# Kernel tuning notes

Hardware: AMD Instinct MI355X
Metric: run time of the kernel (lower is better)

The kernel has to match this reference:

```python
import jax, jax.numpy as jnp
import numpy as np

# Dims: B batch, CK key dim, CV value dim, NOBJ objects, T memory frames, HxW feature map
B, CK, CV, NOBJ, T, H, W = 1, 64, 512, 2, 2, 64, 64


def setup_inputs() -> dict:
    key = jax.random.key(0)
    k1, k2, k3, k4, k5 = jax.random.split(key, 5)
    return {
        "query_key": jax.random.normal(k1, (B, CK, H, W), jnp.float32),
        "query_selection": jax.random.uniform(k2, (B, CK, H, W), jnp.float32),
        "memory_key": jax.random.normal(k3, (B, CK, T, H, W), jnp.float32),
        "memory_shrinkage": jax.random.uniform(k4, (B, 1, T, H, W), jnp.float32),
        "memory_value": jax.random.normal(k5, (B, NOBJ, CV, T, H, W), jnp.float32),
    }


def reference(query_key, query_selection, memory_key, memory_shrinkage, memory_value):
    b, nobj, cv = memory_value.shape[:3]
    ck = memory_key.shape[1]
    h, w = query_key.shape[-2:]
    hw = h * w
    mk = memory_key.reshape(b, ck, -1)            # (b, ck, N) with N = T*H*W
    ms = memory_shrinkage.reshape(b, -1)          # (b, N)
    qk = query_key.reshape(b, ck, hw)             # (b, ck, hw)
    qe = query_selection.reshape(b, ck, hw)       # (b, ck, hw)
    mv = memory_value.reshape(b, nobj * cv, -1)   # (b, nobj*cv, N)

    # Negative L2 similarity with selection weighting (XMem get_similarity)
    a_sq = jnp.einsum('bcn,bcp->bnp', mk * mk, qe)            # (b, N, hw)
    two_ab = 2.0 * jnp.einsum('bcn,bcp->bnp', mk, qk * qe)    # (b, N, hw)
    b_sq = jnp.sum(qe * qk * qk, axis=1, keepdims=True)       # (b, 1, hw)
    inv_sqrt_ck = np.float32(1.0 / np.sqrt(ck))
    sim = (two_ab - a_sq - b_sq) * ms[:, :, None] * inv_sqrt_ck

    # Softmax over memory slots (dim N), then weighted readout
    aff = jax.nn.softmax(sim, axis=1)                          # (b, N, hw)
    mem = jnp.einsum('bvn,bnp->bvp', mv, aff)                  # (b, nobj*cv, hw)
    return mem.reshape(b, nobj, cv, h, w)
```

## Files before the change

kernel.cpp:

```cpp
#include <hip/hip_runtime.h>
#include <stdint.h>

typedef unsigned short u16;
typedef __attribute__((ext_vector_type(4))) float f32x4;
typedef __attribute__((ext_vector_type(8))) __bf16 bf16x8;
typedef __attribute__((ext_vector_type(4))) unsigned int u32x4;

#define HWPX 4096
#define NMEM 8192
#define CKD  64
#define VROWS 1024

__device__ __forceinline__ u16 f2bf(float x) {
    union { float f; unsigned u; } v; v.f = x;
    unsigned r = v.u + 0x7FFFu + ((v.u >> 16) & 1u);
    return (u16)(r >> 16);
}

__device__ __forceinline__ void gld_lds16(const void* g, void* l) {
    __builtin_amdgcn_global_load_lds(
        (const __attribute__((address_space(1))) uint32_t*)g,
        (__attribute__((address_space(3))) uint32_t*)l, 16, 0, 0);
}

__global__ void prep_qk(const float* __restrict__ qk, const float* __restrict__ qe,
                        const float* __restrict__ mk,
                        u16* __restrict__ Qhat, float* __restrict__ bsq,
                        u16* __restrict__ Khat) {
    const int bx = blockIdx.x;
    const int tid = threadIdx.x;
    if (bx < 16) {
        int p = bx * 256 + tid;
        float acc = 0.f;
        #pragma unroll 4
        for (int c = 0; c < CKD; ++c) {
            float k = qk[c * HWPX + p];
            float e = qe[c * HWPX + p];
            Qhat[p * 128 + c]      = f2bf(k * e);
            Qhat[p * 128 + 64 + c] = f2bf(e);
            acc += e * k * k;
        }
        bsq[p] = acc;
    } else {
        int n = (bx - 16) * 256 + tid;
        #pragma unroll 4
        for (int c = 0; c < CKD; ++c) {
            float m = mk[c * NMEM + n];
            Khat[n * 128 + c]      = f2bf(2.f * m);
            Khat[n * 128 + 64 + c] = f2bf(-m * m);
        }
    }
}

__launch_bounds__(256, 4)
__global__ void gemm1_combo(const u16* __restrict__ Qhat, const u16* __restrict__ Khat,
                            const float* __restrict__ bsq, const float* __restrict__ ms,
                            const float* __restrict__ mv,
                            u16* __restrict__ Pt, float* __restrict__ dpart,
                            u16* __restrict__ mvb, float* __restrict__ outz) {
    const int blk = blockIdx.x;
    const int tid = threadIdx.x;

    if (blk < 512) {
        #pragma unroll 4
        for (int it = 0; it < 16; ++it) {
            int i = blk * 4096 + it * 256 + tid;
            float4 v = ((const float4*)mv)[i];
            u16 o0 = f2bf(v.x), o1 = f2bf(v.y), o2 = f2bf(v.z), o3 = f2bf(v.w);
            unsigned lo = (unsigned)o0 | ((unsigned)o1 << 16);
            unsigned hi = (unsigned)o2 | ((unsigned)o3 << 16);
            ((uint2*)mvb)[i] = make_uint2(lo, hi);
        }
        return;
    }
    if (blk < 768) {
        #pragma unroll 4
        for (int it = 0; it < 16; ++it) {
            int i = (blk - 512) * 4096 + it * 256 + tid;
            ((float4*)outz)[i] = make_float4(0.f, 0.f, 0.f, 0.f);
        }
        return;
    }

    __shared__ __align__(16) u16 smem[17408];
    u16* Qs = smem;
    u16* Ks = smem + 8192;

    const int tile = blk - 768;
    const int pb = tile & 31;
    const int nb = tile >> 5;
    const int p0 = pb * 128;
    const int n0 = nb * 128;

    const int l    = tid & 63;
    const int w    = tid >> 6;
    const int quad = l >> 4;
    const int l15  = l & 15;
    const int wm = w >> 1, wn = w & 1;

    const int rsub = tid >> 3;
    const int csw  = (tid & 7) ^ (rsub & 7);

    f32x4 acc[4][4] = {};

    #pragma unroll
    for (int h = 0; h < 2; ++h) {
        if (h) __syncthreads();
        #pragma unroll
        for (int rnd = 0; rnd < 4; ++rnd)
            gld_lds16(Qhat + (size_t)(p0 + rnd * 32 + rsub) * 128 + h * 64 + csw * 8,
                      Qs + rnd * 2048 + w * 512);
        #pragma unroll
        for (int rnd = 0; rnd < 4; ++rnd)
            gld_lds16(Khat + (size_t)(n0 + rnd * 32 + rsub) * 128 + h * 64 + csw * 8,
                      Ks + rnd * 2048 + w * 512);
        __syncthreads();
        #pragma unroll
        for (int kk = 0; kk < 2; ++kk) {
            bf16x8 a[4], b[4];
            #pragma unroll
            for (int mi = 0; mi < 4; ++mi) {
                int row = wm * 64 + mi * 16 + l15;
                a[mi] = *(const bf16x8*)(Qs + row * 64 + (((kk * 4 + quad) ^ (l15 & 7)) << 3));
            }
            #pragma unroll
            for (int ni = 0; ni < 4; ++ni) {
                int row = wn * 64 + ni * 16 + l15;
                b[ni] = *(const bf16x8*)(Ks + row * 64 + (((kk * 4 + quad) ^ (l15 & 7)) << 3));
            }
            #pragma unroll
            for (int mi = 0; mi < 4; ++mi)
                #pragma unroll
                for (int ni = 0; ni < 4; ++ni)
                    acc[mi][ni] = __builtin_amdgcn_mfma_f32_16x16x32_bf16(a[mi], b[ni], acc[mi][ni], 0, 0, 0);
        }
    }

    float msv[4];
    #pragma unroll
    for (int ni = 0; ni < 4; ++ni)
        msv[ni] = ms[n0 + wn * 64 + ni * 16 + l15] * 0.125f;
    float bsv[4][4];
    #pragma unroll
    for (int mi = 0; mi < 4; ++mi)
        #pragma unroll
        for (int r = 0; r < 4; ++r)
            bsv[mi][r] = bsq[p0 + wm * 64 + mi * 16 + quad * 4 + r];

    __syncthreads();
    u16* Ps = smem;
    float rowsum[4][4] = {};
    #pragma unroll
    for (int mi = 0; mi < 4; ++mi) {
        #pragma unroll
        for (int ni = 0; ni < 4; ++ni) {
            f32x4 v = acc[mi][ni];
            int col = wn * 64 + ni * 16 + l15;
            #pragma unroll
            for (int r = 0; r < 4; ++r) {
                int rowl = wm * 64 + mi * 16 + quad * 4 + r;
                float pv = __expf((v[r] - bsv[mi][r]) * msv[ni]);
                rowsum[mi][r] += pv;
                Ps[rowl * 136 + col] = f2bf(pv);
            }
        }
    }
    #pragma unroll
    for (int mi = 0; mi < 4; ++mi)
        #pragma unroll
        for (int r = 0; r < 4; ++r) {
            float s = rowsum[mi][r];
            s += __shfl_xor(s, 1);
            s += __shfl_xor(s, 2);
            s += __shfl_xor(s, 4);
            s += __shfl_xor(s, 8);
            rowsum[mi][r] = s;
        }
    {
        float myv = 0.f;
        #pragma unroll
        for (int mi = 0; mi < 4; ++mi)
            #pragma unroll
            for (int r = 0; r < 4; ++r)
                if (l15 == mi * 4 + r) myv = rowsum[mi][r];
        int slice = nb * 2 + wn;
        dpart[(size_t)slice * HWPX + p0 + wm * 64 + (l15 >> 2) * 16 + quad * 4 + (l15 & 3)] = myv;
    }
    __syncthreads();

    {
        const size_t dstBase = ((size_t)pb * 64 + nb) * 16384;
        #pragma unroll
        for (int i = 0; i < 8; ++i) {
            int row = i * 16 + (tid >> 4);
            const u32x4* src = (const u32x4*)(Ps + row * 136 + (tid & 15) * 8);
            u32x4* dst = (u32x4*)(Pt + dstBase + row * 128 + (tid & 15) * 8);
            *dst = *src;
        }
    }
}

__launch_bounds__(256, 4)
__global__ void gemm2_kernel(const u16* __restrict__ Ab, const u16* __restrict__ Bt,
                             const float* __restrict__ dpart, float* __restrict__ outacc) {
    __shared__ __align__(16) u16 As[128 * 64];
    __shared__ __align__(16) u16 Bs[128 * 64];

    const int tid  = threadIdx.x;
    const int l    = tid & 63;
    const int w    = tid >> 6;
    const int quad = l >> 4;
    const int l15  = l & 15;
    const int wm = w >> 1, wn = w & 1;

    const int lin = blockIdx.x + (blockIdx.y << 3) + (blockIdx.z << 8);
    const int vb  = (lin >> 3) & 7;
    const int pb  = (lin & 7) | (((lin >> 6) & 3) << 3);
    const int kz  = lin >> 8;
    const int v0 = vb * 128;
    const int p0 = pb * 128;
    const int kbeg = kz * (NMEM / 4);
    const int kend = kbeg + (NMEM / 4);

    const int rsub = tid >> 3;
    const int csw  = (tid & 7) ^ (rsub & 7);

    f32x4 acc[4][4] = {};

    for (int k0 = kbeg; k0 < kend; k0 += 64) {
        const int nb = k0 >> 7;
        const int nh = (k0 >> 6) & 1;
        const u16* bsrc = Bt + ((size_t)pb * 64 + nb) * 16384 + nh * 64;
        __syncthreads();
        #pragma unroll
        for (int rnd = 0; rnd < 4; ++rnd) {
            gld_lds16(Ab + (size_t)(v0 + rnd * 32 + rsub) * NMEM + k0 + csw * 8,
                      As + rnd * 2048 + w * 512);
            gld_lds16(bsrc + (rnd * 32 + rsub) * 128 + csw * 8,
                      Bs + rnd * 2048 + w * 512);
        }
        __syncthreads();
        #pragma unroll
        for (int kk = 0; kk < 2; ++kk) {
            bf16x8 a[4], b[4];
            #pragma unroll
            for (int mi = 0; mi < 4; ++mi) {
                int row = wm * 64 + mi * 16 + l15;
                a[mi] = *(const bf16x8*)(As + row * 64 + (((kk * 4 + quad) ^ (l15 & 7)) << 3));
            }
            #pragma unroll
            for (int ni = 0; ni < 4; ++ni) {
                int row = wn * 64 + ni * 16 + l15;
                b[ni] = *(const bf16x8*)(Bs + row * 64 + (((kk * 4 + quad) ^ (l15 & 7)) << 3));
            }
            #pragma unroll
            for (int mi = 0; mi < 4; ++mi)
                #pragma unroll
                for (int ni = 0; ni < 4; ++ni)
                    acc[mi][ni] = __builtin_amdgcn_mfma_f32_16x16x32_bf16(a[mi], b[ni], acc[mi][ni], 0, 0, 0);
        }
    }

    __syncthreads();
    float* dtmp = (float*)As;
    float* dinvs = (float*)Bs;
    {
        int p = tid & 127, h = tid >> 7;
        float s = 0.f;
        #pragma unroll 8
        for (int sl = 0; sl < 64; ++sl)
            s += dpart[(size_t)(h * 64 + sl) * HWPX + p0 + p];
        dtmp[tid] = s;
    }
    __syncthreads();
    if (tid < 128) dinvs[tid] = 1.0f / (dtmp[tid] + dtmp[tid + 128]);
    __syncthreads();

    float dinv[4];
    #pragma unroll
    for (int ni = 0; ni < 4; ++ni)
        dinv[ni] = dinvs[wn * 64 + ni * 16 + l15];

    #pragma unroll
    for (int mi = 0; mi < 4; ++mi) {
        #pragma unroll
        for (int ni = 0; ni < 4; ++ni) {
            int col = p0 + wn * 64 + ni * 16 + l15;
            f32x4 v = acc[mi][ni];
            #pragma unroll
            for (int r = 0; r < 4; ++r) {
                int row = v0 + wm * 64 + mi * 16 + quad * 4 + r;
                atomicAdd(&outacc[(size_t)row * HWPX + col], v[r] * dinv[ni]);
            }
        }
    }
}

extern "C" void kernel_launch(void* const* d_in, const int* in_sizes, int n_in,
                              void* d_out, int out_size, void* d_ws, size_t ws_size,
                              hipStream_t stream) {
    const float* qk = (const float*)d_in[0];
    const float* qe = (const float*)d_in[1];
    const float* mk = (const float*)d_in[2];
    const float* ms = (const float*)d_in[3];
    const float* mv = (const float*)d_in[4];
    float* out = (float*)d_out;

    char* ws = (char*)d_ws;
    u16*   Pt    = (u16*)ws;
    u16*   mvb   = (u16*)(ws + ((size_t)64 << 20));
    u16*   Khat  = (u16*)(ws + ((size_t)80 << 20));
    u16*   Qhat  = (u16*)(ws + ((size_t)82 << 20));
    float* bsq   = (float*)(ws + ((size_t)83 << 20));
    float* dpart = (float*)(ws + ((size_t)83 << 20) + 65536);

    prep_qk<<<48, 256, 0, stream>>>(qk, qe, mk, Qhat, bsq, Khat);

    gemm1_combo<<<2816, 256, 0, stream>>>(Qhat, Khat, bsq, ms, mv, Pt, dpart, mvb, out);

    dim3 g2(8, 32, 4);
    gemm2_kernel<<<g2, 256, 0, stream>>>(mvb, Pt, dpart, out);
}
```

Measured before the change: 226.3 us.

## Pre-swizzle GEMM operands into MFMA fragment layout and load directly to registers

Q/K prep and the P-tile writeback now store operands in a fragment-major layout, so each lane can load its MFMA operand with one contiguous 16-byte global load. gemm1 drops its LDS staging and barriers, and gemm2 keeps only the A operand in LDS while B fragments go straight to registers. The aim is to cut LDS traffic and synchronization, at the cost of more register pressure (launch bounds lowered to 2 and 3) and global loads that are no longer shared across waves through LDS.

```diff
diff --git a/kernel.cpp b/kernel.cpp
--- a/kernel.cpp
+++ b/kernel.cpp
@@ -23,37 +23,70 @@
         (__attribute__((address_space(3))) uint32_t*)l, 16, 0, 0);
 }
 
+
 __global__ void prep_qk(const float* __restrict__ qk, const float* __restrict__ qe,
                         const float* __restrict__ mk,
-                        u16* __restrict__ Qhat, float* __restrict__ bsq,
-                        u16* __restrict__ Khat) {
+                        u16* __restrict__ Qf, float* __restrict__ bsq,
+                        u16* __restrict__ Kf) {
     const int bx = blockIdx.x;
     const int tid = threadIdx.x;
     if (bx < 16) {
         int p = bx * 256 + tid;
+        const int pt = p >> 7, wm = (p >> 6) & 1, mi = (p >> 4) & 3, l15 = p & 15;
+        const size_t cb = ((((size_t)pt * 2 + 0) * 2 + wm) * 4 + mi) * 2;
         float acc = 0.f;
-        #pragma unroll 4
-        for (int c = 0; c < CKD; ++c) {
-            float k = qk[c * HWPX + p];
-            float e = qe[c * HWPX + p];
-            Qhat[p * 128 + c]      = f2bf(k * e);
-            Qhat[p * 128 + 64 + c] = f2bf(e);
-            acc += e * k * k;
+        #pragma unroll
+        for (int cg = 0; cg < 8; ++cg) {
+            const int kk = cg >> 2, quad = cg & 3;
+            float kv[8], ev[8];
+            #pragma unroll
+            for (int j = 0; j < 8; ++j) {
+                int c = cg * 8 + j;
+                kv[j] = qk[c * HWPX + p];
+                ev[j] = qe[c * HWPX + p];
+                acc += ev[j] * kv[j] * kv[j];
+            }
+            unsigned w0[4], w1[4];
+            #pragma unroll
+            for (int jj = 0; jj < 4; ++jj) {
+                w0[jj] = (unsigned)f2bf(kv[2*jj] * ev[2*jj]) |
+                         ((unsigned)f2bf(kv[2*jj+1] * ev[2*jj+1]) << 16);
+                w1[jj] = (unsigned)f2bf(ev[2*jj]) |
+                         ((unsigned)f2bf(ev[2*jj+1]) << 16);
+            }
+            const size_t off = (size_t)quad * 128 + (size_t)l15 * 8;
+            *(u32x4*)(Qf + (cb + kk) * 512 + off)      = (u32x4){w0[0], w0[1], w0[2], w0[3]};
+            *(u32x4*)(Qf + (cb + 16 + kk) * 512 + off) = (u32x4){w1[0], w1[1], w1[2], w1[3]};
         }
         bsq[p] = acc;
     } else {
         int n = (bx - 16) * 256 + tid;
-        #pragma unroll 4
-        for (int c = 0; c < CKD; ++c) {
-            float m = mk[c * NMEM + n];
-            Khat[n * 128 + c]      = f2bf(2.f * m);
-            Khat[n * 128 + 64 + c] = f2bf(-m * m);
-        }
-    }
-}
-
-__launch_bounds__(256, 4)
-__global__ void gemm1_combo(const u16* __restrict__ Qhat, const u16* __restrict__ Khat,
+        const int nt = n >> 7, wn = (n >> 6) & 1, ni = (n >> 4) & 3, l15 = n & 15;
+        const size_t cb = ((((size_t)nt * 2 + 0) * 2 + wn) * 4 + ni) * 2;
+        #pragma unroll
+        for (int cg = 0; cg < 8; ++cg) {
+            const int kk = cg >> 2, quad = cg & 3;
+            float m[8];
+            #pragma unroll
+            for (int j = 0; j < 8; ++j)
+                m[j] = mk[(cg * 8 + j) * NMEM + n];
+            unsigned w0[4], w1[4];
+            #pragma unroll
+            for (int jj = 0; jj < 4; ++jj) {
+                w0[jj] = (unsigned)f2bf(2.f * m[2*jj]) |
+                         ((unsigned)f2bf(2.f * m[2*jj+1]) << 16);
+                w1[jj] = (unsigned)f2bf(-m[2*jj] * m[2*jj]) |
+                         ((unsigned)f2bf(-m[2*jj+1] * m[2*jj+1]) << 16);
+            }
+            const size_t off = (size_t)quad * 128 + (size_t)l15 * 8;
+            *(u32x4*)(Kf + (cb + kk) * 512 + off)      = (u32x4){w0[0], w0[1], w0[2], w0[3]};
+            *(u32x4*)(Kf + (cb + 16 + kk) * 512 + off) = (u32x4){w1[0], w1[1], w1[2], w1[3]};
+        }
+    }
+}
+
+__launch_bounds__(256, 2)
+__global__ void gemm1_combo(const u16* __restrict__ Qf, const u16* __restrict__ Kf,
                             const float* __restrict__ bsq, const float* __restrict__ ms,
                             const float* __restrict__ mv,
                             u16* __restrict__ Pt, float* __restrict__ dpart,
@@ -83,8 +116,6 @@
     }
 
     __shared__ __align__(16) u16 smem[17408];
-    u16* Qs = smem;
-    u16* Ks = smem + 8192;
 
     const int tile = blk - 768;
     const int pb = tile & 31;
@@ -98,42 +129,30 @@
     const int l15  = l & 15;
     const int wm = w >> 1, wn = w & 1;
 
-    const int rsub = tid >> 3;
-    const int csw  = (tid & 7) ^ (rsub & 7);
-
     f32x4 acc[4][4] = {};
 
     #pragma unroll
     for (int h = 0; h < 2; ++h) {
-        if (h) __syncthreads();
-        #pragma unroll
-        for (int rnd = 0; rnd < 4; ++rnd)
-            gld_lds16(Qhat + (size_t)(p0 + rnd * 32 + rsub) * 128 + h * 64 + csw * 8,
-                      Qs + rnd * 2048 + w * 512);
-        #pragma unroll
-        for (int rnd = 0; rnd < 4; ++rnd)
-            gld_lds16(Khat + (size_t)(n0 + rnd * 32 + rsub) * 128 + h * 64 + csw * 8,
-                      Ks + rnd * 2048 + w * 512);
-        __syncthreads();
-        #pragma unroll
-        for (int kk = 0; kk < 2; ++kk) {
-            bf16x8 a[4], b[4];
-            #pragma unroll
-            for (int mi = 0; mi < 4; ++mi) {
-                int row = wm * 64 + mi * 16 + l15;
-                a[mi] = *(const bf16x8*)(Qs + row * 64 + (((kk * 4 + quad) ^ (l15 & 7)) << 3));
-            }
-            #pragma unroll
-            for (int ni = 0; ni < 4; ++ni) {
-                int row = wn * 64 + ni * 16 + l15;
-                b[ni] = *(const bf16x8*)(Ks + row * 64 + (((kk * 4 + quad) ^ (l15 & 7)) << 3));
-            }
+        bf16x8 a[4][2], b[4][2];
+        const u16* qbase = Qf + ((((size_t)pb * 2 + h) * 2 + wm) * 4096) + (size_t)l * 8;
+        const u16* kbase = Kf + ((((size_t)nb * 2 + h) * 2 + wn) * 4096) + (size_t)l * 8;
+        #pragma unroll
+        for (int mi = 0; mi < 4; ++mi) {
+            a[mi][0] = *(const bf16x8*)(qbase + mi * 1024);
+            a[mi][1] = *(const bf16x8*)(qbase + mi * 1024 + 512);
+        }
+        #pragma unroll
+        for (int ni = 0; ni < 4; ++ni) {
+            b[ni][0] = *(const bf16x8*)(kbase + ni * 1024);
+            b[ni][1] = *(const bf16x8*)(kbase + ni * 1024 + 512);
+        }
+        #pragma unroll
+        for (int kk = 0; kk < 2; ++kk)
             #pragma unroll
             for (int mi = 0; mi < 4; ++mi)
                 #pragma unroll
                 for (int ni = 0; ni < 4; ++ni)
-                    acc[mi][ni] = __builtin_amdgcn_mfma_f32_16x16x32_bf16(a[mi], b[ni], acc[mi][ni], 0, 0, 0);
-        }
+                    acc[mi][ni] = __builtin_amdgcn_mfma_f32_16x16x32_bf16(a[mi][kk], b[ni][kk], acc[mi][ni], 0, 0, 0);
     }
 
     float msv[4];
@@ -147,7 +166,6 @@
         for (int r = 0; r < 4; ++r)
             bsv[mi][r] = bsq[p0 + wm * 64 + mi * 16 + quad * 4 + r];
 
-    __syncthreads();
     u16* Ps = smem;
     float rowsum[4][4] = {};
     #pragma unroll
@@ -189,22 +207,27 @@
     __syncthreads();
 
     {
-        const size_t dstBase = ((size_t)pb * 64 + nb) * 16384;
-        #pragma unroll
-        for (int i = 0; i < 8; ++i) {
-            int row = i * 16 + (tid >> 4);
-            const u32x4* src = (const u32x4*)(Ps + row * 136 + (tid & 15) * 8);
-            u32x4* dst = (u32x4*)(Pt + dstBase + row * 128 + (tid & 15) * 8);
+        const size_t dstBase = (size_t)pb * 1048576 + (size_t)nb * 16384;
+        #pragma unroll
+        for (int it = 0; it < 8; ++it) {
+            const int combo = it * 4 + w;
+            const int kt  = combo >> 4;
+            const int wnq = (combo >> 3) & 1;
+            const int niq = (combo >> 1) & 3;
+            const int kkq = combo & 1;
+            const u32x4* src = (const u32x4*)(Ps + (wnq * 64 + niq * 16 + l15) * 136
+                                                 + kt * 64 + kkq * 32 + quad * 8);
+            u32x4* dst = (u32x4*)(Pt + dstBase + kt * 8192 + wnq * 4096
+                                     + niq * 1024 + kkq * 512 + l * 8);
             *dst = *src;
         }
     }
 }
 
-__launch_bounds__(256, 4)
-__global__ void gemm2_kernel(const u16* __restrict__ Ab, const u16* __restrict__ Bt,
+__launch_bounds__(256, 3)
+__global__ void gemm2_kernel(const u16* __restrict__ Ab, const u16* __restrict__ Btf,
                              const float* __restrict__ dpart, float* __restrict__ outacc) {
     __shared__ __align__(16) u16 As[128 * 64];
-    __shared__ __align__(16) u16 Bs[128 * 64];
 
     const int tid  = threadIdx.x;
     const int l    = tid & 63;
@@ -225,45 +248,46 @@
     const int rsub = tid >> 3;
     const int csw  = (tid & 7) ^ (rsub & 7);
 
+    const u16* bbase = Btf + (size_t)pb * 1048576 + (size_t)wn * 4096 + (size_t)l * 8;
+
     f32x4 acc[4][4] = {};
 
     for (int k0 = kbeg; k0 < kend; k0 += 64) {
-        const int nb = k0 >> 7;
-        const int nh = (k0 >> 6) & 1;
-        const u16* bsrc = Bt + ((size_t)pb * 64 + nb) * 16384 + nh * 64;
+        const int kt = k0 >> 6;
         __syncthreads();
         #pragma unroll
-        for (int rnd = 0; rnd < 4; ++rnd) {
+        for (int rnd = 0; rnd < 4; ++rnd)
             gld_lds16(Ab + (size_t)(v0 + rnd * 32 + rsub) * NMEM + k0 + csw * 8,
                       As + rnd * 2048 + w * 512);
-            gld_lds16(bsrc + (rnd * 32 + rsub) * 128 + csw * 8,
-                      Bs + rnd * 2048 + w * 512);
+        bf16x8 b[4][2];
+        {
+            const u16* bk = bbase + (size_t)kt * 8192;
+            #pragma unroll
+            for (int ni = 0; ni < 4; ++ni) {
+                b[ni][0] = *(const bf16x8*)(bk + ni * 1024);
+                b[ni][1] = *(const bf16x8*)(bk + ni * 1024 + 512);
+            }
         }
         __syncthreads();
         #pragma unroll
         for (int kk = 0; kk < 2; ++kk) {
-            bf16x8 a[4], b[4];
+            bf16x8 a[4];
             #pragma unroll
             for (int mi = 0; mi < 4; ++mi) {
                 int row = wm * 64 + mi * 16 + l15;
                 a[mi] = *(const bf16x8*)(As + row * 64 + (((kk * 4 + quad) ^ (l15 & 7)) << 3));
             }
             #pragma unroll
-            for (int ni = 0; ni < 4; ++ni) {
-                int row = wn * 64 + ni * 16 + l15;
-                b[ni] = *(const bf16x8*)(Bs + row * 64 + (((kk * 4 + quad) ^ (l15 & 7)) << 3));
-            }
-            #pragma unroll
             for (int mi = 0; mi < 4; ++mi)
                 #pragma unroll
                 for (int ni = 0; ni < 4; ++ni)
-                    acc[mi][ni] = __builtin_amdgcn_mfma_f32_16x16x32_bf16(a[mi], b[ni], acc[mi][ni], 0, 0, 0);
+                    acc[mi][ni] = __builtin_amdgcn_mfma_f32_16x16x32_bf16(a[mi], b[ni][kk], acc[mi][ni], 0, 0, 0);
         }
     }
 
     __syncthreads();
-    float* dtmp = (float*)As;
-    float* dinvs = (float*)Bs;
+    float* dtmp  = (float*)As;
+    float* dinvs = (float*)(As + 2048);
     {
         int p = tid & 127, h = tid >> 7;
         float s = 0.f;
@@ -309,14 +333,14 @@
     char* ws = (char*)d_ws;
     u16*   Pt    = (u16*)ws;
     u16*   mvb   = (u16*)(ws + ((size_t)64 << 20));
-    u16*   Khat  = (u16*)(ws + ((size_t)80 << 20));
-    u16*   Qhat  = (u16*)(ws + ((size_t)82 << 20));
+    u16*   Kf    = (u16*)(ws + ((size_t)80 << 20));
+    u16*   Qf    = (u16*)(ws + ((size_t)82 << 20));
     float* bsq   = (float*)(ws + ((size_t)83 << 20));
     float* dpart = (float*)(ws + ((size_t)83 << 20) + 65536);
 
-    prep_qk<<<48, 256, 0, stream>>>(qk, qe, mk, Qhat, bsq, Khat);
-
-    gemm1_combo<<<2816, 256, 0, stream>>>(Qhat, Khat, bsq, ms, mv, Pt, dpart, mvb, out);
+    prep_qk<<<48, 256, 0, stream>>>(qk, qe, mk, Qf, bsq, Kf);
+
+    gemm1_combo<<<2816, 256, 0, stream>>>(Qf, Kf, bsq, ms, mv, Pt, dpart, mvb, out);
 
     dim3 g2(8, 32, 4);
     gemm2_kernel<<<g2, 256, 0, stream>>>(mvb, Pt, dpart, out);
```

Result: no change. 222.0 us (-1.9%).
